# Optimization experiments

Measured on AMD Instinct MI355X. Metric: run time of the kernel, lower is better.

The kernel has to match this reference:

```python
import jax, jax.numpy as jnp
import numpy as np

# module hyperparams (from init_kwargs)
D = 1024      # dim
T = 16        # num_tiles
TD = D // T   # tile_dim = 64
K = 4         # num_wormholes (<= T-1)
TEMP = 0.1    # routing temperature
LN_EPS = 1e-5


def setup_inputs() -> dict:
    key = jax.random.key(0)
    ks = jax.random.split(key, 8)
    B, S = 4, 4096
    x = jax.random.normal(ks[0], (B, S, D), jnp.float32)
    # LayerNorm params
    gamma = jnp.ones((D,), jnp.float32)
    beta = jnp.zeros((D,), jnp.float32)
    # tile_query / tile_key: Linear(TD, TD)
    def lin(k, out_f, in_f):
        w = jax.random.normal(k, (out_f, in_f), jnp.float32) / np.sqrt(in_f).astype(np.float32)
        return w
    Wq = lin(ks[1], TD, TD); bq = jnp.zeros((TD,), jnp.float32)
    Wk = lin(ks[2], TD, TD); bk = jnp.zeros((TD,), jnp.float32)
    # processor: Linear((1+K)*TD, 2*TD) -> GELU -> Linear(2*TD, TD)
    W1 = lin(ks[3], 2 * TD, (1 + K) * TD); b1 = jnp.zeros((2 * TD,), jnp.float32)
    W2 = lin(ks[4], TD, 2 * TD); b2 = jnp.zeros((TD,), jnp.float32)
    return {"x": x, "gamma": gamma, "beta": beta, "Wq": Wq, "bq": bq,
            "Wk": Wk, "bk": bk, "W1": W1, "b1": b1, "W2": W2, "b2": b2}


def _l2norm(v):
    # F.normalize(dim=-1), eps=1e-12
    n = jnp.linalg.norm(v, axis=-1, keepdims=True)
    return v / jnp.maximum(n, 1e-12)


def reference(x, gamma, beta, Wq, bq, Wk, bk, W1, b1, W2, b2):
    B, S, Dd = x.shape
    # LayerNorm
    mu = jnp.mean(x, axis=-1, keepdims=True)
    var = jnp.mean(jnp.square(x - mu), axis=-1, keepdims=True)
    xn = (x - mu) * jax.lax.rsqrt(var + LN_EPS) * gamma + beta
    x_tiles = xn.reshape(B, S, T, TD)                      # [B,S,T,td]
    tile_repr = jnp.mean(x_tiles, axis=1)                  # [B,T,td]
    q = _l2norm(tile_repr @ Wq.T + bq)                     # [B,T,td]
    k = _l2norm(tile_repr @ Wk.T + bk)
    scores = jnp.einsum('btd,bud->btu', q, k)              # [B,T,T]
    scores = jnp.where(jnp.eye(T, dtype=bool), jnp.float32(-1e9), scores)
    topk_scores, routes = jax.lax.top_k(scores / TEMP, K)  # [B,T,K]
    # wormhole gather: gathered[b,s,t,k] = x_tiles[b,s,routes[b,t,k]]
    def gather_one(xt, r):   # xt:[S,T,td], r:[T,K]
        g = jnp.take(xt, r.reshape(-1), axis=1)            # [S,T*K,td]
        return g.reshape(xt.shape[0], T, K, TD)
    gathered = jax.vmap(gather_one)(x_tiles, routes)       # [B,S,T,K,td]
    combined = jnp.concatenate([x_tiles, gathered.reshape(B, S, T, K * TD)], axis=-1)
    h = jax.nn.gelu(combined @ W1.T + b1, approximate=False)
    out_tiles = h @ W2.T + b2                              # [B,S,T,td]
    return x + out_tiles.reshape(B, S, Dd)
```

## Files before the change

### kernel.cpp

```cpp
#include <hip/hip_runtime.h>
#include <hip/hip_bf16.h>

typedef float floatx4 __attribute__((ext_vector_type(4)));
typedef __bf16 bf16x8 __attribute__((ext_vector_type(8)));

__device__ __forceinline__ unsigned short f2bf(float f){
  unsigned u = __builtin_bit_cast(unsigned, f);
  u += 0x7fffu + ((u >> 16) & 1u);
  return (unsigned short)(u >> 16);
}
__device__ __forceinline__ unsigned pk2(float a, float b){
  return (unsigned)f2bf(a) | ((unsigned)f2bf(b) << 16);
}
__device__ __forceinline__ float wred64(float v){
  v += __shfl_xor(v, 32); v += __shfl_xor(v, 16); v += __shfl_xor(v, 8);
  v += __shfl_xor(v, 4);  v += __shfl_xor(v, 2);  v += __shfl_xor(v, 1);
  return v;
}
__device__ __forceinline__ float gelu_f(float v){
  float u = v * v;
  float y = v * __builtin_fmaf(u, 0.0356774081f, 0.7978845608f);
  float a = __builtin_fabsf(y);
  float t = __builtin_amdgcn_exp2f(-2.8853900818f * a);
  float th = (1.0f - t) * __builtin_amdgcn_rcpf(1.0f + t);
  return 0.5f * (v + __builtin_fabsf(v) * th);
}

__global__ __launch_bounds__(256) void wk_ln_part(const float* __restrict__ x,
    const float* __restrict__ gm, const float* __restrict__ bt, float* __restrict__ part){
  __shared__ float red[4][1024];
  const int tid = threadIdx.x, w = tid >> 6, lane = tid & 63;
  const int blk = blockIdx.x;
  floatx4 gv[4], bv[4];
#pragma unroll
  for (int j = 0; j < 4; ++j){
    gv[j] = *(const floatx4*)(gm + j*256 + lane*4);
    bv[j] = *(const floatx4*)(bt + j*256 + lane*4);
  }
  floatx4 acc[4];
#pragma unroll
  for (int j = 0; j < 4; ++j){ acc[j][0]=0.f; acc[j][1]=0.f; acc[j][2]=0.f; acc[j][3]=0.f; }
  const int row0 = blk*32 + w*8;
#pragma unroll 2
  for (int r = 0; r < 8; ++r){
    const float* xr = x + (size_t)(row0 + r) * 1024;
    floatx4 xv[4];
#pragma unroll
    for (int j = 0; j < 4; ++j) xv[j] = *(const floatx4*)(xr + j*256 + lane*4);
    float s = 0.f, s2 = 0.f;
#pragma unroll
    for (int j = 0; j < 4; ++j)
#pragma unroll
      for (int e = 0; e < 4; ++e){ float v = xv[j][e]; s += v; s2 += v*v; }
    s = wred64(s); s2 = wred64(s2);
    const float mu = s * (1.0f/1024.0f);
    const float rs = rsqrtf(s2 * (1.0f/1024.0f) - mu*mu + 1e-5f);
#pragma unroll
    for (int j = 0; j < 4; ++j)
#pragma unroll
      for (int e = 0; e < 4; ++e)
        acc[j][e] += (xv[j][e] - mu) * rs * gv[j][e] + bv[j][e];
  }
#pragma unroll
  for (int j = 0; j < 4; ++j) *(floatx4*)(&red[w][j*256 + lane*4]) = acc[j];
  __syncthreads();
  const int p = tid * 4;
  floatx4 s0 = *(const floatx4*)(&red[0][p]);
  floatx4 s1 = *(const floatx4*)(&red[1][p]);
  floatx4 s2v = *(const floatx4*)(&red[2][p]);
  floatx4 s3 = *(const floatx4*)(&red[3][p]);
  *(floatx4*)(part + (size_t)blk*1024 + p) = s0 + s1 + s2v + s3;
}

__global__ __launch_bounds__(256) void wk_reduce(const float* __restrict__ part, float* __restrict__ trep,
    const float* __restrict__ W1, const float* __restrict__ W2,
    unsigned short* __restrict__ W1bf, unsigned short* __restrict__ W2bf){
  __shared__ float red[4][64];
  const int j = blockIdx.x, b = j >> 4, chunk = j & 15;
  const int t = threadIdx.x, po = t & 63, part4 = t >> 6;
  const int p = chunk*64 + po;
  float s = 0.f;
  for (int i = 0; i < 32; ++i) s += part[(size_t)(b*128 + part4*32 + i)*1024 + p];
  red[part4][po] = s;
  __syncthreads();
  if (t < 64) trep[b*1024 + chunk*64 + t] = red[0][t] + red[1][t] + red[2][t] + red[3][t];
  for (int i = j*256 + t; i < 128*320; i += 64*256) W1bf[i] = f2bf(W1[i]);
  for (int i = j*256 + t; i < 64*128;  i += 64*256) W2bf[i] = f2bf(W2[i]);
}

__global__ __launch_bounds__(256) void wk_route(const float* __restrict__ trep,
    const float* __restrict__ Wq, const float* __restrict__ bq,
    const float* __restrict__ Wk, const float* __restrict__ bk, int* __restrict__ routes){
  __shared__ float tr[4096];
  __shared__ float qnt[4096], knt[4096];
  __shared__ float redq[4][64], redk[4][64];
  __shared__ float scs[1024];
  const int t = threadIdx.x, w = t >> 6, lane = t & 63;
  for (int i = t; i < 4096; i += 256){
    const int row = i >> 6, jw = i & 63;
    tr[row*64 + (jw ^ ((row & 7) << 2))] = trep[i] * (1.0f/4096.0f);
  }
  __syncthreads();
  float trv[64];
  {
    const int sw = (lane & 7) << 2;
#pragma unroll
    for (int j = 0; j < 16; ++j){
      const floatx4 v = *(const floatx4*)(&tr[lane*64 + ((j*4) ^ sw)]);
      trv[j*4+0]=v[0]; trv[j*4+1]=v[1]; trv[j*4+2]=v[2]; trv[j*4+3]=v[3];
    }
  }
  float qv[16], kv[16], sq = 0.f, sk = 0.f;
#pragma unroll 4
  for (int dd = 0; dd < 16; ++dd){
    const int d = __builtin_amdgcn_readfirstlane(w*16 + dd);
    const float* wqr = Wq + d*64;
    const float* wkr = Wk + d*64;
    float aq = bq[d], ak = bk[d];
#pragma unroll
    for (int j = 0; j < 64; ++j){
      aq = __builtin_fmaf(wqr[j], trv[j], aq);
      ak = __builtin_fmaf(wkr[j], trv[j], ak);
    }
    qv[dd] = aq; kv[dd] = ak; sq += aq*aq; sk += ak*ak;
  }
  redq[w][lane] = sq; redk[w][lane] = sk;
  __syncthreads();
  const float nq = sqrtf(redq[0][lane]+redq[1][lane]+redq[2][lane]+redq[3][lane]);
  const float nk = sqrtf(redk[0][lane]+redk[1][lane]+redk[2][lane]+redk[3][lane]);
  const float iq = 1.0f / fmaxf(nq, 1e-12f), ik = 1.0f / fmaxf(nk, 1e-12f);
#pragma unroll
  for (int dd = 0; dd < 16; ++dd){
    qnt[(w*16 + dd)*64 + lane] = qv[dd]*iq;
    knt[(w*16 + dd)*64 + lane] = kv[dd]*ik;
  }
  __syncthreads();
  {
    const int sidx = t*4, b = sidx >> 8, tt = (sidx >> 4) & 15, uu0 = sidx & 15;
    const int qp = b*16 + tt;
    float qrow[64];
#pragma unroll
    for (int dd = 0; dd < 64; ++dd) qrow[dd] = qnt[dd*64 + qp];
#pragma unroll
    for (int e = 0; e < 4; ++e){
      const int kp = b*16 + uu0 + e;
      float s = 0.f;
#pragma unroll
      for (int dd = 0; dd < 64; ++dd) s = __builtin_fmaf(qrow[dd], knt[dd*64 + kp], s);
      scs[qp*16 + uu0 + e] = s;
    }
  }
  __syncthreads();
  if (t < 64){
    const int tt = t & 15;
    float sc[16];
#pragma unroll
    for (int u = 0; u < 16; ++u) sc[u] = scs[t*16 + u];
    sc[tt] = -3.0e38f;
    for (int kk = 0; kk < 4; ++kk){
      float best = -3.4e38f; int bi = 0;
#pragma unroll
      for (int u = 0; u < 16; ++u) if (sc[u] > best){ best = sc[u]; bi = u; }
      routes[t*4 + kk] = bi;
      sc[bi] = -3.4e38f;
    }
  }
}

#define MFMA16(accv, av, bbv) accv = __builtin_amdgcn_mfma_f32_16x16x32_bf16(av, bbv, accv, 0, 0, 0)

__global__ __launch_bounds__(256, 2) void wk_main(const float* __restrict__ x,
    const float* __restrict__ gm, const float* __restrict__ bt,
    const float* __restrict__ b1, const float* __restrict__ b2p,
    const unsigned short* __restrict__ W1bf, const unsigned short* __restrict__ W2bf,
    const int* __restrict__ routes, float* __restrict__ out){
  __shared__ char sm[40960];
  const int tid = threadIdx.x, w = tid >> 6, lane = tid & 63;
  const int c = lane & 15, g = lane >> 4;
  char* xnb = sm;
  char* Hb  = sm + 8192;
  char* W2s = sm + 24576;
#pragma unroll
  for (int q = 0; q < 4; ++q){
    const int cid = tid*4 + q, row = cid >> 4, k16 = cid & 15;
    *(int4*)(W2s + row*256 + ((k16*16) ^ ((row & 7) << 4))) = *(const int4*)(W2bf + row*128 + k16*8);
  }
  bf16x8 w1f[2][10];
#pragma unroll
  for (int mi = 0; mi < 2; ++mi)
#pragma unroll
    for (int kk = 0; kk < 10; ++kk)
      w1f[mi][kk] = *(const bf16x8*)(W1bf + ((2*w + mi)*16 + c)*320 + kk*32 + g*8);
  floatx4 gvv[4], bvv[4];
#pragma unroll
  for (int j = 0; j < 4; ++j){
    gvv[j] = *(const floatx4*)(gm + j*256 + lane*4);
    bvv[j] = *(const floatx4*)(bt + j*256 + lane*4);
  }
  floatx4 b1v[2];
#pragma unroll
  for (int mi = 0; mi < 2; ++mi) b1v[mi] = *(const floatx4*)(b1 + (2*w + mi)*16 + g*4);
  float b2v[4];
#pragma unroll
  for (int nn = 0; nn < 4; ++nn) b2v[nn] = b2p[nn*16 + c];
  const int bbat = blockIdx.x >> 7;
  const int4 rt4 = *(const int4*)(routes + (bbat*16 + c)*4);
  const int rts[5] = {c, rt4.x, rt4.y, rt4.z, rt4.w};
  const int swc = (c & 7) << 4;
  const int g16 = g * 16;

#pragma unroll 1
  for (int q = 0; q < 8; ++q){
    const int row = blockIdx.x*32 + q*4 + w;
    const float* xr = x + (size_t)row * 1024;
    floatx4 xv[4];
#pragma unroll
    for (int j = 0; j < 4; ++j) xv[j] = *(const floatx4*)(xr + j*256 + lane*4);
    float s = 0.f, s2 = 0.f;
#pragma unroll
    for (int j = 0; j < 4; ++j)
#pragma unroll
      for (int e = 0; e < 4; ++e){ float v = xv[j][e]; s += v; s2 += v*v; }
    s = wred64(s); s2 = wred64(s2);
    const float mu = s * (1.0f/1024.0f);
    const float rs = rsqrtf(s2 * (1.0f/1024.0f) - mu*mu + 1e-5f);
#pragma unroll
    for (int j = 0; j < 4; ++j){
      floatx4 xn = (xv[j] - mu) * rs * gvv[j] + bvv[j];
      uint2 pv; pv.x = pk2(xn[0], xn[1]); pv.y = pk2(xn[2], xn[3]);
      const int o = j*512 + lane*8;
      *(uint2*)(xnb + w*2048 + (o ^ (((o >> 7) & 7) << 4))) = pv;
    }
    __syncthreads();
    floatx4 acc[4][2];
#pragma unroll
    for (int r = 0; r < 4; ++r)
#pragma unroll
      for (int mi = 0; mi < 2; ++mi){ acc[r][mi][0]=0.f; acc[r][mi][1]=0.f; acc[r][mi][2]=0.f; acc[r][mi][3]=0.f; }
#pragma unroll
    for (int kk = 0; kk < 10; ++kk){
      const int s_ = rts[kk >> 1];
      const int baddr = (s_*128 + (kk & 1)*64 + g16) ^ ((s_ & 7) << 4);
      bf16x8 bfr[4];
#pragma unroll
      for (int r = 0; r < 4; ++r) bfr[r] = *(const bf16x8*)(xnb + r*2048 + baddr);
#pragma unroll
      for (int r = 0; r < 4; ++r)
#pragma unroll
        for (int mi = 0; mi < 2; ++mi)
          MFMA16(acc[r][mi], w1f[mi][kk], bfr[r]);
    }
#pragma unroll
    for (int r = 0; r < 4; ++r)
#pragma unroll
      for (int mi = 0; mi < 2; ++mi){
        floatx4 z = acc[r][mi] + b1v[mi];
        uint2 pv; pv.x = pk2(gelu_f(z[0]), gelu_f(z[1])); pv.y = pk2(gelu_f(z[2]), gelu_f(z[3]));
        *(uint2*)(Hb + r*4096 + c*256 + ((((2*w + mi)*32) + g*8) ^ swc)) = pv;
      }
    __syncthreads();
    floatx4 a2c[4];
#pragma unroll
    for (int n = 0; n < 4; ++n){ a2c[n][0]=0.f; a2c[n][1]=0.f; a2c[n][2]=0.f; a2c[n][3]=0.f; }
#pragma unroll
    for (int k2 = 0; k2 < 4; ++k2){
      const bf16x8 a2 = *(const bf16x8*)(Hb + w*4096 + c*256 + (((k2*64) + g16) ^ swc));
#pragma unroll
      for (int n = 0; n < 4; ++n){
        const bf16x8 b2f = *(const bf16x8*)(W2s + (n*16 + c)*256 + (((k2*64) + g16) ^ swc));
        MFMA16(a2c[n], a2, b2f);
      }
    }
    float* Ob = (float*)(Hb + w*4096);
#pragma unroll
    for (int n = 0; n < 4; ++n)
#pragma unroll
      for (int reg = 0; reg < 4; ++reg){
        const int orow = g*4 + reg;
        Ob[orow*64 + ((n*16 + c) ^ ((orow & 7) << 2))] = a2c[n][reg] + b2v[n];
      }
    float* op = out + (size_t)row * 1024;
#pragma unroll
    for (int j = 0; j < 4; ++j){
      const int orow = j*4 + g;
      const floatx4 ov = *(const floatx4*)(Ob + orow*64 + ((c*4) ^ ((orow & 7) << 2)));
      *(floatx4*)(op + j*256 + lane*4) = ov + xv[j];
    }
    __syncthreads();
  }
}

extern "C" void kernel_launch(void* const* d_in, const int* in_sizes, int n_in,
                              void* d_out, int out_size, void* d_ws, size_t ws_size,
                              hipStream_t stream){
  const float* x  = (const float*)d_in[0];
  const float* gm = (const float*)d_in[1];
  const float* bt = (const float*)d_in[2];
  const float* Wq = (const float*)d_in[3];
  const float* bq = (const float*)d_in[4];
  const float* Wk = (const float*)d_in[5];
  const float* bk = (const float*)d_in[6];
  const float* W1 = (const float*)d_in[7];
  const float* b1 = (const float*)d_in[8];
  const float* W2 = (const float*)d_in[9];
  const float* b2 = (const float*)d_in[10];
  float* out = (float*)d_out;
  char* ws = (char*)d_ws;
  float* part = (float*)ws;
  float* trep = part + 512*1024;
  int*   routes = (int*)(trep + 4096);
  unsigned short* W1bf = (unsigned short*)(ws + 2114560);
  unsigned short* W2bf = (unsigned short*)(ws + 2196480);

  wk_ln_part<<<512, 256, 0, stream>>>(x, gm, bt, part);
  wk_reduce<<<64, 256, 0, stream>>>(part, trep, W1, W2, W1bf, W2bf);
  wk_route<<<1, 256, 0, stream>>>(trep, Wq, bq, Wk, bk, routes);
  wk_main<<<512, 256, 0, stream>>>(x, gm, bt, b1, b2, W1bf, W2bf, routes, out);
}
```

Baseline: 94.45 us.

## Fuse partial reduction and routing into one per-batch kernel, move weight casts

Removes the separate reduce kernel by merging the cross-block partial-sum reduction into the routing kernel, which now runs one block per batch instead of a single block. The bf16 weight conversion moves into the first LayerNorm-partial kernel. This cuts one launch and the intermediate trep buffer and spreads the routing work over four blocks. In exchange, each routing block serially reads 128 partial rows, and most lanes sit idle in the projection stage.

```diff
diff --git a/kernel.cpp b/kernel.cpp
--- a/kernel.cpp
+++ b/kernel.cpp
@@ -27,10 +27,16 @@
 }
 
 __global__ __launch_bounds__(256) void wk_ln_part(const float* __restrict__ x,
-    const float* __restrict__ gm, const float* __restrict__ bt, float* __restrict__ part){
+    const float* __restrict__ gm, const float* __restrict__ bt, float* __restrict__ part,
+    const float* __restrict__ W1, const float* __restrict__ W2,
+    unsigned short* __restrict__ W1bf, unsigned short* __restrict__ W2bf){
   __shared__ float red[4][1024];
   const int tid = threadIdx.x, w = tid >> 6, lane = tid & 63;
   const int blk = blockIdx.x;
+  if (blk < 64){
+    for (int i = blk*256 + tid; i < 128*320; i += 64*256) W1bf[i] = f2bf(W1[i]);
+    for (int i = blk*256 + tid; i < 64*128;  i += 64*256) W2bf[i] = f2bf(W2[i]);
+  }
   floatx4 gv[4], bv[4];
 #pragma unroll
   for (int j = 0; j < 4; ++j){
@@ -72,41 +78,35 @@
   *(floatx4*)(part + (size_t)blk*1024 + p) = s0 + s1 + s2v + s3;
 }
 
-__global__ __launch_bounds__(256) void wk_reduce(const float* __restrict__ part, float* __restrict__ trep,
-    const float* __restrict__ W1, const float* __restrict__ W2,
-    unsigned short* __restrict__ W1bf, unsigned short* __restrict__ W2bf){
-  __shared__ float red[4][64];
-  const int j = blockIdx.x, b = j >> 4, chunk = j & 15;
-  const int t = threadIdx.x, po = t & 63, part4 = t >> 6;
-  const int p = chunk*64 + po;
-  float s = 0.f;
-  for (int i = 0; i < 32; ++i) s += part[(size_t)(b*128 + part4*32 + i)*1024 + p];
-  red[part4][po] = s;
-  __syncthreads();
-  if (t < 64) trep[b*1024 + chunk*64 + t] = red[0][t] + red[1][t] + red[2][t] + red[3][t];
-  for (int i = j*256 + t; i < 128*320; i += 64*256) W1bf[i] = f2bf(W1[i]);
-  for (int i = j*256 + t; i < 64*128;  i += 64*256) W2bf[i] = f2bf(W2[i]);
-}
-
-__global__ __launch_bounds__(256) void wk_route(const float* __restrict__ trep,
+__global__ __launch_bounds__(256) void wk_redroute(const float* __restrict__ part,
     const float* __restrict__ Wq, const float* __restrict__ bq,
     const float* __restrict__ Wk, const float* __restrict__ bk, int* __restrict__ routes){
-  __shared__ float tr[4096];
-  __shared__ float qnt[4096], knt[4096];
-  __shared__ float redq[4][64], redk[4][64];
-  __shared__ float scs[1024];
-  const int t = threadIdx.x, w = t >> 6, lane = t & 63;
-  for (int i = t; i < 4096; i += 256){
-    const int row = i >> 6, jw = i & 63;
-    tr[row*64 + (jw ^ ((row & 7) << 2))] = trep[i] * (1.0f/4096.0f);
-  }
-  __syncthreads();
+  __shared__ float tr[1024];
+  __shared__ float qnt[1024], knt[1024];
+  __shared__ float redq[4][16], redk[4][16];
+  __shared__ float scs[256];
+  const int t = threadIdx.x, w = t >> 6, lane = t & 63, b = blockIdx.x;
+  {
+    floatx4 sg[4];
+#pragma unroll
+    for (int g = 0; g < 4; ++g){
+      sg[g][0]=0.f; sg[g][1]=0.f; sg[g][2]=0.f; sg[g][3]=0.f;
+      for (int i = 0; i < 32; ++i)
+        sg[g] += *(const floatx4*)(part + (size_t)(b*128 + g*32 + i)*1024 + t*4);
+    }
+    const floatx4 tot = ((sg[0] + sg[1]) + sg[2]) + sg[3];
+    const floatx4 tv = tot * (1.0f/4096.0f);
+    const int row = t >> 4, jw0 = (t & 15)*4;
+    *(floatx4*)(&tr[row*64 + (jw0 ^ ((row & 7) << 2))]) = tv;
+  }
+  __syncthreads();
+  const int pair = lane & 15;
   float trv[64];
   {
-    const int sw = (lane & 7) << 2;
+    const int sw = (pair & 7) << 2;
 #pragma unroll
     for (int j = 0; j < 16; ++j){
-      const floatx4 v = *(const floatx4*)(&tr[lane*64 + ((j*4) ^ sw)]);
+      const floatx4 v = *(const floatx4*)(&tr[pair*64 + ((j*4) ^ sw)]);
       trv[j*4+0]=v[0]; trv[j*4+1]=v[1]; trv[j*4+2]=v[2]; trv[j*4+3]=v[3];
     }
   }
@@ -124,44 +124,44 @@
     }
     qv[dd] = aq; kv[dd] = ak; sq += aq*aq; sk += ak*ak;
   }
-  redq[w][lane] = sq; redk[w][lane] = sk;
-  __syncthreads();
-  const float nq = sqrtf(redq[0][lane]+redq[1][lane]+redq[2][lane]+redq[3][lane]);
-  const float nk = sqrtf(redk[0][lane]+redk[1][lane]+redk[2][lane]+redk[3][lane]);
+  if (lane < 16){ redq[w][pair] = sq; redk[w][pair] = sk; }
+  __syncthreads();
+  const float nq = sqrtf(redq[0][pair]+redq[1][pair]+redq[2][pair]+redq[3][pair]);
+  const float nk = sqrtf(redk[0][pair]+redk[1][pair]+redk[2][pair]+redk[3][pair]);
   const float iq = 1.0f / fmaxf(nq, 1e-12f), ik = 1.0f / fmaxf(nk, 1e-12f);
-#pragma unroll
-  for (int dd = 0; dd < 16; ++dd){
-    qnt[(w*16 + dd)*64 + lane] = qv[dd]*iq;
-    knt[(w*16 + dd)*64 + lane] = kv[dd]*ik;
-  }
-  __syncthreads();
-  {
-    const int sidx = t*4, b = sidx >> 8, tt = (sidx >> 4) & 15, uu0 = sidx & 15;
-    const int qp = b*16 + tt;
+  if (lane < 16){
+#pragma unroll
+    for (int dd = 0; dd < 16; ++dd){
+      qnt[(w*16 + dd)*16 + pair] = qv[dd]*iq;
+      knt[(w*16 + dd)*16 + pair] = kv[dd]*ik;
+    }
+  }
+  __syncthreads();
+  if (t < 64){
+    const int tt = t >> 2, uu0 = (t & 3)*4;
     float qrow[64];
 #pragma unroll
-    for (int dd = 0; dd < 64; ++dd) qrow[dd] = qnt[dd*64 + qp];
+    for (int dd = 0; dd < 64; ++dd) qrow[dd] = qnt[dd*16 + tt];
 #pragma unroll
     for (int e = 0; e < 4; ++e){
-      const int kp = b*16 + uu0 + e;
+      const int kp = uu0 + e;
       float s = 0.f;
 #pragma unroll
-      for (int dd = 0; dd < 64; ++dd) s = __builtin_fmaf(qrow[dd], knt[dd*64 + kp], s);
-      scs[qp*16 + uu0 + e] = s;
-    }
-  }
-  __syncthreads();
-  if (t < 64){
-    const int tt = t & 15;
+      for (int dd = 0; dd < 64; ++dd) s = __builtin_fmaf(qrow[dd], knt[dd*16 + kp], s);
+      scs[tt*16 + uu0 + e] = s;
+    }
+  }
+  __syncthreads();
+  if (t < 16){
     float sc[16];
 #pragma unroll
     for (int u = 0; u < 16; ++u) sc[u] = scs[t*16 + u];
-    sc[tt] = -3.0e38f;
+    sc[t] = -3.0e38f;
     for (int kk = 0; kk < 4; ++kk){
       float best = -3.4e38f; int bi = 0;
 #pragma unroll
       for (int u = 0; u < 16; ++u) if (sc[u] > best){ best = sc[u]; bi = u; }
-      routes[t*4 + kk] = bi;
+      routes[(b*16 + t)*4 + kk] = bi;
       sc[bi] = -3.4e38f;
     }
   }
@@ -307,13 +307,11 @@
   float* out = (float*)d_out;
   char* ws = (char*)d_ws;
   float* part = (float*)ws;
-  float* trep = part + 512*1024;
-  int*   routes = (int*)(trep + 4096);
+  int*   routes = (int*)(ws + 2097152);
   unsigned short* W1bf = (unsigned short*)(ws + 2114560);
   unsigned short* W2bf = (unsigned short*)(ws + 2196480);
 
-  wk_ln_part<<<512, 256, 0, stream>>>(x, gm, bt, part);
-  wk_reduce<<<64, 256, 0, stream>>>(part, trep, W1, W2, W1bf, W2bf);
-  wk_route<<<1, 256, 0, stream>>>(trep, Wq, bq, Wk, bk, routes);
+  wk_ln_part<<<512, 256, 0, stream>>>(x, gm, bt, part, W1, W2, W1bf, W2bf);
+  wk_redroute<<<4, 256, 0, stream>>>(part, Wq, bq, Wk, bk, routes);
   wk_main<<<512, 256, 0, stream>>>(x, gm, bt, b1, b2, W1bf, W2bf, routes, out);
 }
```

Result: no change. 95.21 us (+0.8%).
